# Optimization experiments

Measured on AMD Instinct MI355X. Metric: run time of the kernel, lower is better.

The kernel has to match this reference:

```python
import jax, jax.numpy as jnp
import numpy as np

B, D = 4096, 512
STEPS = 50
LR, B1, B2, EPS = 0.01, 0.9, 0.999, 1e-8  # torch.optim.Adam defaults with lr=0.01


def setup_inputs() -> dict:
    key = jax.random.key(0)
    k1, k2, k3, k4 = jax.random.split(key, 4)
    s = jax.random.normal(k1, (B, D), dtype=jnp.float32)
    target_confidence = jax.random.uniform(k2, (B, 1), dtype=jnp.float32)
    # nn.Linear(style_dim, 1) init: U(-1/sqrt(D), 1/sqrt(D))
    lim = 1.0 / np.sqrt(D)
    W = jax.random.uniform(k3, (1, D), dtype=jnp.float32, minval=-lim, maxval=lim)
    b = jax.random.uniform(k4, (1,), dtype=jnp.float32, minval=-lim, maxval=lim)
    return {"s": s, "target_confidence": target_confidence, "W": W, "b": b}


def reference(s, target_confidence, W, b):
    # loss(x) = mse(sigmoid(x W^T + b), t) + l1(x, s); grad taken w.r.t. x only.
    def loss_fn(x):
        p = jax.nn.sigmoid(x @ W.T + b)                      # [B, 1]
        mse = jnp.mean((p - target_confidence) ** 2)
        d = x - s
        # stop_gradient(sign) so d|d|/dx = sign(d), with sign(0) = 0 (matches torch l1_loss subgradient)
        l1 = jnp.mean(jax.lax.stop_gradient(jnp.sign(d)) * d)
        return mse + l1

    grad_fn = jax.grad(loss_fn)

    def adam_step(carry, _):
        x, m, v, t = carry
        g = grad_fn(x)
        t = t + 1.0
        m = B1 * m + (1.0 - B1) * g
        v = B2 * v + (1.0 - B2) * g * g
        m_hat = m / (1.0 - B1 ** t)
        v_hat = v / (1.0 - B2 ** t)
        x = x - LR * m_hat / (jnp.sqrt(v_hat) + EPS)
        return (x, m, v, t), None

    init = (s, jnp.zeros_like(s), jnp.zeros_like(s), jnp.float32(0.0))
    (adjusted_s, _, _, _), _ = jax.lax.scan(adam_step, init, None, length=STEPS)
    return adjusted_s
```

## Files before the change

### kernel.cpp

```cpp
#include <hip/hip_runtime.h>

#define B_ 4096
#define D_ 512
#define STEPS_ 50

#define DPP_ADD(x, ctrl) \
    ((x) + __int_as_float(__builtin_amdgcn_update_dpp( \
        0, __float_as_int(x), (ctrl), 0xf, 0xf, true)))

__device__ __forceinline__ float row16_sum(float x) {
    x = DPP_ADD(x, 0x111);
    x = DPP_ADD(x, 0x112);
    x = DPP_ADD(x, 0x114);
    x = DPP_ADD(x, 0x118);
    return x;
}

__device__ __forceinline__ float grp_bcast15(float x, int vsel) {
    return __int_as_float(__builtin_amdgcn_ds_bpermute(vsel, __float_as_int(x)));
}

__device__ __forceinline__ float coef_from_z(float z, float t) {
    const float e = __expf(-z);
    const float q = __builtin_amdgcn_rcpf(1.0f + e);
    return (q - t) * (e * (q * q));
}

__global__ __launch_bounds__(64, 1) void adam_rows_kernel(
    const float* __restrict__ s,
    const float* __restrict__ tgt,
    const float* __restrict__ W,
    const float* __restrict__ bias_p,
    float* __restrict__ out)
{
    const int lane = threadIdx.x;
    const int grp  = lane >> 4;
    const int j    = lane & 15;
    const int row  = blockIdx.x * 4 + grp;
    const int vsel = ((lane & 48) | 15) << 2;

    float vAn;
    {
        const float t1 = (float)(lane + 1);
        const float p1 = exp2f(t1 * -0.15200309344505f);
        const float p2 = exp2f(t1 * -0.00144345345258f);
        vAn = (-0.0316227766017f * __builtin_amdgcn_sqrtf(1.0f - p2)) *
              __builtin_amdgcn_rcpf(1.0f - p1);
    }

    const float c_mse = 0x1p-11f;
    const float K     = 2048.0f;
    const float c_l1  = 0x1p-21f;

    const float4* W4  = (const float4*)W;
    const float4* sr4 = (const float4*)(s + (size_t)row * D_);

    float ws[32], dl[32], M[32], V[32];
#pragma unroll
    for (int q = 0; q < 8; ++q) {
        const float4 w = W4[j + 16 * q];
        ws[4*q+0] = w.x * c_mse; ws[4*q+1] = w.y * c_mse;
        ws[4*q+2] = w.z * c_mse; ws[4*q+3] = w.w * c_mse;
    }

    float vzb;
    {
        float a0 = 0.0f, a1 = 0.0f, a2 = 0.0f, a3 = 0.0f;
#pragma unroll
        for (int q = 0; q < 8; ++q) {
            const float4 e = sr4[j + 16 * q];
            a0 = fmaf(e.x, ws[4*q+0], a0);
            a1 = fmaf(e.y, ws[4*q+1], a1);
            a2 = fmaf(e.z, ws[4*q+2], a2);
            a3 = fmaf(e.w, ws[4*q+3], a3);
        }
        vzb = fmaf(K, row16_sum((a0 + a1) + (a2 + a3)), bias_p[0]);
    }
    const float vtg = tgt[row];

    float vc;

    {
        const float An0 =
            __int_as_float(__builtin_amdgcn_readlane(__float_as_int(vAn), 0));
        vc = grp_bcast15(coef_from_z(vzb, vtg), vsel);
        float a0 = 0.0f, a1 = 0.0f, a2 = 0.0f, a3 = 0.0f;
#pragma unroll
        for (int k = 0; k < 32; ++k) {
            const float g = vc * ws[k];
            M[k] = g;
            V[k] = fmaf(g, g, 1e-30f);
            dl[k] = (An0 * g) * __builtin_amdgcn_rsqf(V[k]);
            float* acc = (k & 2) ? ((k & 1) ? &a3 : &a2) : ((k & 1) ? &a1 : &a0);
            *acc = fmaf(dl[k], ws[k], *acc);
        }
        const float vz = fmaf(K, row16_sum((a0 + a1) + (a2 + a3)), vzb);
        vc = grp_bcast15(coef_from_z(vz, vtg), vsel);
    }

#pragma unroll 1
    for (int step = 1; step < STEPS_; ++step) {
        const float An =
            __int_as_float(__builtin_amdgcn_readlane(__float_as_int(vAn), step));
        float a0 = 0.0f, a1 = 0.0f, a2 = 0.0f, a3 = 0.0f;
#pragma unroll
        for (int k = 0; k < 32; ++k) {
            const float g = fmaf(vc, ws[k], __builtin_copysignf(c_l1, dl[k]));
            M[k] = fmaf(0.9f,   M[k], g);
            V[k] = fmaf(0.999f, V[k], g * g);
            dl[k] = fmaf(An * M[k], __builtin_amdgcn_rsqf(V[k]), dl[k]);
            float* acc = (k & 2) ? ((k & 1) ? &a3 : &a2) : ((k & 1) ? &a1 : &a0);
            *acc = fmaf(dl[k], ws[k], *acc);
        }
        if (step != STEPS_ - 1) {
            const float vz = fmaf(K, row16_sum((a0 + a1) + (a2 + a3)), vzb);
            vc = grp_bcast15(coef_from_z(vz, vtg), vsel);
        }
    }

    float4* orow = (float4*)(out + (size_t)row * D_);
#pragma unroll
    for (int q = 0; q < 8; ++q) {
        const float4 e = sr4[j + 16 * q];
        float4 o = {e.x + dl[4*q+0], e.y + dl[4*q+1],
                    e.z + dl[4*q+2], e.w + dl[4*q+3]};
        orow[j + 16 * q] = o;
    }
}

extern "C" void kernel_launch(void* const* d_in, const int* in_sizes, int n_in,
                              void* d_out, int out_size, void* d_ws, size_t ws_size,
                              hipStream_t stream) {
    const float* s    = (const float*)d_in[0];
    const float* tgt  = (const float*)d_in[1];
    const float* W    = (const float*)d_in[2];
    const float* bias = (const float*)d_in[3];
    float* out = (float*)d_out;

    adam_rows_kernel<<<dim3(B_ / 4), dim3(64), 0, stream>>>(s, tgt, W, bias, out);
}
```

Baseline: 91.11 us.

## Map one row per wavefront with packed float2 math and full-wave reduction

Each row now gets a whole 64-lane wavefront (8 elements per lane) instead of 16 lanes per row (32 elements per lane), with 256-thread blocks covering 4 rows. The per-element Adam update uses two-wide float vectors so the compiler can emit packed FP32 instructions. The row dot product becomes a full-wave DPP reduction plus a readlane, replacing the 16-lane reduction and bpermute broadcast. This shortens each lane's serial chain and lowers register pressure, at the cost of more wavefronts and a longer reduction on every step.

```diff
diff --git a/kernel.cpp b/kernel.cpp
--- a/kernel.cpp
+++ b/kernel.cpp
@@ -4,20 +4,20 @@
 #define D_ 512
 #define STEPS_ 50
 
+typedef float v2f __attribute__((ext_vector_type(2)));
+
 #define DPP_ADD(x, ctrl) \
     ((x) + __int_as_float(__builtin_amdgcn_update_dpp( \
         0, __float_as_int(x), (ctrl), 0xf, 0xf, true)))
 
-__device__ __forceinline__ float row16_sum(float x) {
+__device__ __forceinline__ float wave64_sum(float x) {
     x = DPP_ADD(x, 0x111);
     x = DPP_ADD(x, 0x112);
     x = DPP_ADD(x, 0x114);
     x = DPP_ADD(x, 0x118);
-    return x;
-}
-
-__device__ __forceinline__ float grp_bcast15(float x, int vsel) {
-    return __int_as_float(__builtin_amdgcn_ds_bpermute(vsel, __float_as_int(x)));
+    x = DPP_ADD(x, 0x142);
+    x = DPP_ADD(x, 0x143);
+    return __int_as_float(__builtin_amdgcn_readlane(__float_as_int(x), 63));
 }
 
 __device__ __forceinline__ float coef_from_z(float z, float t) {
@@ -26,18 +26,17 @@
     return (q - t) * (e * (q * q));
 }
 
-__global__ __launch_bounds__(64, 1) void adam_rows_kernel(
+__device__ __forceinline__ v2f mk2(float a, float b) { v2f r; r.x = a; r.y = b; return r; }
+
+__global__ __launch_bounds__(256, 4) void adam_row_kernel(
     const float* __restrict__ s,
     const float* __restrict__ tgt,
     const float* __restrict__ W,
     const float* __restrict__ bias_p,
     float* __restrict__ out)
 {
-    const int lane = threadIdx.x;
-    const int grp  = lane >> 4;
-    const int j    = lane & 15;
-    const int row  = blockIdx.x * 4 + grp;
-    const int vsel = ((lane & 48) | 15) << 2;
+    const int lane = threadIdx.x & 63;
+    const int row  = blockIdx.x * 4 + (threadIdx.x >> 6);
 
     float vAn;
     {
@@ -55,77 +54,79 @@
     const float4* W4  = (const float4*)W;
     const float4* sr4 = (const float4*)(s + (size_t)row * D_);
 
-    float ws[32], dl[32], M[32], V[32];
-#pragma unroll
-    for (int q = 0; q < 8; ++q) {
-        const float4 w = W4[j + 16 * q];
-        ws[4*q+0] = w.x * c_mse; ws[4*q+1] = w.y * c_mse;
-        ws[4*q+2] = w.z * c_mse; ws[4*q+3] = w.w * c_mse;
+    const float4 w0 = W4[lane], w1 = W4[lane + 64];
+    const float4 e0 = sr4[lane], e1 = sr4[lane + 64];
+
+    v2f ws[4], sv[4], M[4], V[4], dl[4];
+    ws[0] = mk2(w0.x, w0.y) * c_mse;  ws[1] = mk2(w0.z, w0.w) * c_mse;
+    ws[2] = mk2(w1.x, w1.y) * c_mse;  ws[3] = mk2(w1.z, w1.w) * c_mse;
+    sv[0] = mk2(e0.x, e0.y);          sv[1] = mk2(e0.z, e0.w);
+    sv[2] = mk2(e1.x, e1.y);          sv[3] = mk2(e1.z, e1.w);
+
+    float zb;
+    {
+        v2f a = sv[0] * ws[0];
+        a = sv[1] * ws[1] + a;
+        a = sv[2] * ws[2] + a;
+        a = sv[3] * ws[3] + a;
+        zb = fmaf(K, wave64_sum(a.x + a.y), bias_p[0]);
     }
+    const float tg = tgt[row];
 
-    float vzb;
-    {
-        float a0 = 0.0f, a1 = 0.0f, a2 = 0.0f, a3 = 0.0f;
-#pragma unroll
-        for (int q = 0; q < 8; ++q) {
-            const float4 e = sr4[j + 16 * q];
-            a0 = fmaf(e.x, ws[4*q+0], a0);
-            a1 = fmaf(e.y, ws[4*q+1], a1);
-            a2 = fmaf(e.z, ws[4*q+2], a2);
-            a3 = fmaf(e.w, ws[4*q+3], a3);
-        }
-        vzb = fmaf(K, row16_sum((a0 + a1) + (a2 + a3)), bias_p[0]);
-    }
-    const float vtg = tgt[row];
-
-    float vc;
+    float vc = coef_from_z(zb, tg);
 
     {
-        const float An0 =
-            __int_as_float(__builtin_amdgcn_readlane(__float_as_int(vAn), 0));
-        vc = grp_bcast15(coef_from_z(vzb, vtg), vsel);
-        float a0 = 0.0f, a1 = 0.0f, a2 = 0.0f, a3 = 0.0f;
+        const float An0 = __int_as_float(
+            __builtin_amdgcn_readlane(__float_as_int(vAn), 0));
+        v2f acc = mk2(0.0f, 0.0f);
 #pragma unroll
-        for (int k = 0; k < 32; ++k) {
-            const float g = vc * ws[k];
+        for (int k = 0; k < 4; ++k) {
+            const v2f g = vc * ws[k];
             M[k] = g;
-            V[k] = fmaf(g, g, 1e-30f);
-            dl[k] = (An0 * g) * __builtin_amdgcn_rsqf(V[k]);
-            float* acc = (k & 2) ? ((k & 1) ? &a3 : &a2) : ((k & 1) ? &a1 : &a0);
-            *acc = fmaf(dl[k], ws[k], *acc);
+            V[k] = g * g + 1e-30f;
+            v2f r;
+            r.x = __builtin_amdgcn_rsqf(V[k].x);
+            r.y = __builtin_amdgcn_rsqf(V[k].y);
+            dl[k] = (An0 * g) * r;
+            acc = dl[k] * ws[k] + acc;
         }
-        const float vz = fmaf(K, row16_sum((a0 + a1) + (a2 + a3)), vzb);
-        vc = grp_bcast15(coef_from_z(vz, vtg), vsel);
+        const float z = fmaf(K, wave64_sum(acc.x + acc.y), zb);
+        vc = coef_from_z(z, tg);
     }
 
 #pragma unroll 1
     for (int step = 1; step < STEPS_; ++step) {
-        const float An =
-            __int_as_float(__builtin_amdgcn_readlane(__float_as_int(vAn), step));
-        float a0 = 0.0f, a1 = 0.0f, a2 = 0.0f, a3 = 0.0f;
+        const float An = __int_as_float(
+            __builtin_amdgcn_readlane(__float_as_int(vAn), step));
+        v2f acc = mk2(0.0f, 0.0f);
 #pragma unroll
-        for (int k = 0; k < 32; ++k) {
-            const float g = fmaf(vc, ws[k], __builtin_copysignf(c_l1, dl[k]));
-            M[k] = fmaf(0.9f,   M[k], g);
-            V[k] = fmaf(0.999f, V[k], g * g);
-            dl[k] = fmaf(An * M[k], __builtin_amdgcn_rsqf(V[k]), dl[k]);
-            float* acc = (k & 2) ? ((k & 1) ? &a3 : &a2) : ((k & 1) ? &a1 : &a0);
-            *acc = fmaf(dl[k], ws[k], *acc);
+        for (int k = 0; k < 4; ++k) {
+            v2f sgn;
+            sgn.x = __builtin_copysignf(c_l1, dl[k].x);
+            sgn.y = __builtin_copysignf(c_l1, dl[k].y);
+            const v2f g = vc * ws[k] + sgn;
+            M[k] = 0.9f * M[k] + g;
+            V[k] = 0.999f * V[k] + g * g;
+            v2f r;
+            r.x = __builtin_amdgcn_rsqf(V[k].x);
+            r.y = __builtin_amdgcn_rsqf(V[k].y);
+            dl[k] = (An * M[k]) * r + dl[k];
+            acc = dl[k] * ws[k] + acc;
         }
         if (step != STEPS_ - 1) {
-            const float vz = fmaf(K, row16_sum((a0 + a1) + (a2 + a3)), vzb);
-            vc = grp_bcast15(coef_from_z(vz, vtg), vsel);
+            const float z = fmaf(K, wave64_sum(acc.x + acc.y), zb);
+            vc = coef_from_z(z, tg);
         }
     }
 
-    float4* orow = (float4*)(out + (size_t)row * D_);
-#pragma unroll
-    for (int q = 0; q < 8; ++q) {
-        const float4 e = sr4[j + 16 * q];
-        float4 o = {e.x + dl[4*q+0], e.y + dl[4*q+1],
-                    e.z + dl[4*q+2], e.w + dl[4*q+3]};
-        orow[j + 16 * q] = o;
-    }
+    float4* o4 = (float4*)(out + (size_t)row * D_);
+    float4 o0, o1;
+    o0.x = sv[0].x + dl[0].x; o0.y = sv[0].y + dl[0].y;
+    o0.z = sv[1].x + dl[1].x; o0.w = sv[1].y + dl[1].y;
+    o1.x = sv[2].x + dl[2].x; o1.y = sv[2].y + dl[2].y;
+    o1.z = sv[3].x + dl[3].x; o1.w = sv[3].y + dl[3].y;
+    o4[lane]      = o0;
+    o4[lane + 64] = o1;
 }
 
 extern "C" void kernel_launch(void* const* d_in, const int* in_sizes, int n_in,
@@ -137,5 +138,5 @@
     const float* bias = (const float*)d_in[3];
     float* out = (float*)d_out;
 
-    adam_rows_kernel<<<dim3(B_ / 4), dim3(64), 0, stream>>>(s, tgt, W, bias, out);
+    adam_row_kernel<<<dim3(B_ / 4), dim3(256), 0, stream>>>(s, tgt, W, bias, out);
 }
```

After: 93.60 us. +2.7%, slower.
